# Kernel optimization log

Measured on AMD Instinct MI355X. Metric: run time of the kernel, lower is better.

The kernel has to match this reference:

```python
import jax, jax.numpy as jnp
import numpy as np
from jax import lax

NUM_CLASSES = 5
K_MAX = 5
PROTO_DIM = 32
MARGIN = 1.0
ANCHOR_STRENGTH = 1.0
LAMBDA_COMPACT = 0.1
MAX_ANCHORS = 2048
KMEANS_ITERS = 5
EPS = 1e-12


def _normalize(x, axis=-1):
    return x / jnp.sqrt(jnp.sum(x * x, axis=axis, keepdims=True) + EPS)


def _cdist(a, b):
    # Euclidean distance matrix (n, m) via the squared-norm expansion.
    d2 = (jnp.sum(a * a, 1)[:, None] + jnp.sum(b * b, 1)[None, :] - 2.0 * (a @ b.T))
    return jnp.sqrt(jnp.maximum(d2, 0.0))


def _class_centroids(feats, mask, key):
    # feats: (N, D) L2-normalized; mask: (N,) bool selecting this class's voxels.
    N, D = feats.shape
    w = mask.astype(feats.dtype)
    cnt = w.sum()
    mean = (feats * w[:, None]).sum(0) / jnp.maximum(cnt, 1.0)

    def kmeans(_):
        k_init, k_fb = jax.random.split(key)
        # random init: K distinct masked points (gumbel top-k == randperm sample)
        g0 = jax.random.gumbel(k_init, (N,))
        _, init_idx = lax.top_k(jnp.where(mask, g0, -jnp.inf), K_MAX)
        cent0 = feats[init_idx]
        # fallback random masked points for empty clusters, one set per iter
        g2 = jax.random.gumbel(k_fb, (KMEANS_ITERS, N))
        fb_idx = jax.vmap(lambda s: lax.top_k(jnp.where(mask, s, -jnp.inf), K_MAX)[1])(g2)

        def body(cent, fb):
            d = _cdist(feats, cent)                       # (N, K)
            assign = jnp.argmin(d, axis=1)
            onehot = ((assign[:, None] == jnp.arange(K_MAX)[None, :]) & mask[:, None]).astype(feats.dtype)
            counts = onehot.sum(0)                        # (K,)
            sums = onehot.T @ feats                       # (K, D)
            newc = sums / jnp.maximum(counts, 1.0)[:, None]
            newc = jnp.where(counts[:, None] > 0, newc, feats[fb])
            return newc, None

        cent, _ = lax.scan(body, cent0, fb_idx)
        return _normalize(cent)

    def mean_rep(_):
        return jnp.tile(mean[None, :], (K_MAX, 1))

    cent = lax.cond(cnt >= K_MAX, kmeans, mean_rep, None)
    return _normalize(cent), cnt


def _loss_triplet(feats, prototypes, pseudo_masks, gt_masks, labeled_batch):
    B, Df, Zf, Yf, Xf = feats.shape
    N = B * Zf * Yf * Xf
    feats_flat = _normalize(jnp.transpose(feats, (0, 2, 3, 4, 1)).reshape(N, Df))
    # masks are already at feature resolution -> nearest interp is identity
    gt_flat = gt_masks.reshape(-1)
    pseudo_flat = pseudo_masks.reshape(-1)
    protos = _normalize(prototypes)                       # (C, K, D)
    key = jax.random.key(42)

    # ---- anchor loss: match prototypes to per-class kmeans centroids ----
    anchor_loss = jnp.float32(0.0)
    anchor_cnt = jnp.float32(0.0)
    for i in range(int(labeled_batch.shape[0])):
        c = labeled_batch[i]
        c_safe = jnp.clip(c, 0, NUM_CLASSES - 1)
        cmask = gt_flat == c
        cent, cnt = _class_centroids(feats_flat, cmask, jax.random.fold_in(key, i))
        valid = ((c != 0) & (c < NUM_CLASSES) & (cnt > 0)).astype(jnp.float32)
        loss_c = jnp.mean((protos[c_safe] - cent) ** 2)
        anchor_loss = anchor_loss + valid * loss_c
        anchor_cnt = anchor_cnt + valid
    anchor_loss = anchor_loss / jnp.maximum(anchor_cnt, 1.0)

    # ---- compactness: unbiased variance across the K prototypes per class ----
    compact_loss = jnp.var(protos[1:], axis=1, ddof=1).mean(axis=1).sum()

    # ---- triplet loss over pseudo-labeled anchors ----
    amask = pseudo_flat > 0
    ga = jax.random.gumbel(jax.random.fold_in(key, 1000), (N,))
    top_s, aidx = lax.top_k(jnp.where(amask, ga, -jnp.inf), MAX_ANCHORS)
    sel_valid = jnp.isfinite(top_s)                        # padding if < MAX_ANCHORS anchors
    a_feats = feats_flat[aidx]                             # (A, D)
    a_labels = jnp.clip(pseudo_flat[aidx], 0, NUM_CLASSES - 1)

    CK = NUM_CLASSES * K_MAX
    protos_flat = protos.reshape(CK, Df)
    col_cls = jnp.arange(CK) // K_MAX
    own = col_cls[None, :] == a_labels[:, None]            # (A, CK)

    sim = a_feats @ protos_flat.T
    pos_idx = jnp.argmax(jnp.where(own, sim, -jnp.inf), axis=1)
    pos_vecs = protos_flat[pos_idx]

    d_all = _cdist(a_feats, protos_flat)                   # (A, CK)
    pos_d = jnp.min(jnp.where(own, d_all, jnp.inf), axis=1)
    neg = ~own
    semi = neg & (d_all > pos_d[:, None]) & (d_all < pos_d[:, None] + MARGIN)
    g1 = jax.random.gumbel(jax.random.fold_in(key, 2000), (MAX_ANCHORS, CK))
    g2 = jax.random.gumbel(jax.random.fold_in(key, 2001), (MAX_ANCHORS, CK))
    idx_semi = jnp.argmax(jnp.where(semi, g1, -jnp.inf), axis=1)
    idx_rand = jnp.argmax(jnp.where(neg, g2, -jnp.inf), axis=1)
    neg_idx = jnp.where(semi.any(axis=1), idx_semi, idx_rand)
    neg_vecs = protos_flat[neg_idx]

    aN, pN, nN = _normalize(a_feats), _normalize(pos_vecs), _normalize(neg_vecs)
    d_pos = jnp.sqrt(jnp.sum((aN - pN) ** 2, axis=1) + EPS)
    d_neg = jnp.sqrt(jnp.sum((aN - nN) ** 2, axis=1) + EPS)
    wA = (sel_valid & (a_labels != 0)).astype(jnp.float32)
    proto_loss = jnp.sum(jax.nn.softplus(d_pos - d_neg + MARGIN) * wA) / jnp.maximum(wA.sum(), 1.0)

    return proto_loss + ANCHOR_STRENGTH * anchor_loss + LAMBDA_COMPACT * compact_loss


def setup_inputs() -> dict:
    key = jax.random.key(0)
    k1, k2, k3, k4 = jax.random.split(key, 4)
    B, Z = 4, 64
    feats = jax.random.normal(k1, (B, PROTO_DIM, Z, Z, Z), dtype=jnp.float32)
    protos = jax.random.normal(k2, (NUM_CLASSES, K_MAX, PROTO_DIM), dtype=jnp.float32)
    protos = _normalize(protos)
    pseudo_masks = jax.random.randint(k3, (B, Z, Z, Z), 0, NUM_CLASSES, dtype=jnp.int32)
    gt_masks = jax.random.randint(k4, (B, Z, Z, Z), 0, NUM_CLASSES, dtype=jnp.int32)
    labeled_batch = jnp.array([1, 2, 3, 4], dtype=jnp.int32)
    return {"feats": feats, "prototypes": protos, "pseudo_masks": pseudo_masks,
            "gt_masks": gt_masks, "labeled_batch": labeled_batch}


def reference(feats, prototypes, pseudo_masks, gt_masks, labeled_batch):
    return _loss_triplet(feats, prototypes, pseudo_masks, gt_masks, labeled_batch)
```

## Files before the change

### kernel.cpp

```cpp
#include <hip/hip_runtime.h>
#include <stdint.h>

typedef unsigned int u32;
typedef unsigned long long u64;

#define NCLS 5
#define KMX 5
#define DD 32
#define LBN 4
#define KIT 5
#define MAXA 2048
#define CKK 25
#define NBLKA 256
#define SCPAD 36
#define PSTRIDE 680
#define ACAP 4096
#define UKTHR ((1u << 23) + 1u - (1u << 15))
#define FTINY 1.17549435e-38f

struct RKeys {
  u32 ki[LBN][2];
  u32 kf[LBN][2];
  u32 k1000[2];
  u32 k2000[2];
  u32 k2001[2];
};

struct SelState {
  u32 prefix1, rank1, prefix21, rank2, pivot_sv, target, M, ncand, ncand2;
};

__host__ __device__ inline void tf2x32(u32 k0, u32 k1, u32 x0, u32 x1, u32* o0, u32* o1) {
  u32 ks2 = k0 ^ k1 ^ 0x1BD11BDAu;
  u32 ks[3] = {k0, k1, ks2};
  x0 += k0; x1 += k1;
  const int rotA[4] = {13, 15, 26, 6};
  const int rotB[4] = {17, 29, 16, 24};
#pragma unroll
  for (int g = 0; g < 5; ++g) {
#pragma unroll
    for (int j = 0; j < 4; ++j) {
      int r = (g & 1) ? rotB[j] : rotA[j];
      x0 += x1;
      x1 = (x1 << r) | (x1 >> (32 - r));
      x1 ^= x0;
    }
    x0 += ks[(g + 1) % 3];
    x1 += ks[(g + 2) % 3] + (u32)(g + 1);
  }
  *o0 = x0; *o1 = x1;
}

__device__ inline u32 jax_ukey(u32 k0, u32 k1, u32 half, u32 idx) {
  bool hi = (idx >= half);
  u32 c0 = hi ? (idx - half) : idx;
  u32 c1 = hi ? idx : (idx + half);
  u32 o0, o1;
  tf2x32(k0, k1, c0, c1, &o0, &o1);
  u32 bits = hi ? o1 : o0;
  return (bits >> 9) + 1u;
}

#define INS5(kk, a0, a1, a2, a3, a4) do { u64 _k = (kk); \
  if (_k > a4) { a4 = _k; u64 _t; \
    if (a4 > a3) { _t = a3; a3 = a4; a4 = _t; } \
    if (a3 > a2) { _t = a2; a2 = a3; a3 = _t; } \
    if (a2 > a1) { _t = a1; a1 = a2; a2 = _t; } \
    if (a1 > a0) { _t = a0; a0 = a1; a1 = _t; } } } while (0)

#define WMERGE5(off, a0, a1, a2, a3, a4) do { \
  u64 r0 = __shfl_xor(a0, off, 64), r1 = __shfl_xor(a1, off, 64), \
      r2 = __shfl_xor(a2, off, 64), r3 = __shfl_xor(a3, off, 64), \
      r4 = __shfl_xor(a4, off, 64); \
  INS5(r0, a0, a1, a2, a3, a4); INS5(r1, a0, a1, a2, a3, a4); \
  INS5(r2, a0, a1, a2, a3, a4); INS5(r3, a0, a1, a2, a3, a4); \
  INS5(r4, a0, a1, a2, a3, a4); } while (0)

#define WMERGE_ALL(a0,a1,a2,a3,a4) do { \
  WMERGE5(32,a0,a1,a2,a3,a4); WMERGE5(16,a0,a1,a2,a3,a4); WMERGE5(8,a0,a1,a2,a3,a4); \
  WMERGE5(4,a0,a1,a2,a3,a4); WMERGE5(2,a0,a1,a2,a3,a4); WMERGE5(1,a0,a1,a2,a3,a4); } while (0)

__device__ inline float rsum32(float v) {
#pragma unroll
  for (int o = 16; o; o >>= 1) v += __shfl_xor(v, o, 32);
  return v;
}

__device__ inline float rsum64(float v) {
#pragma unroll
  for (int o = 32; o; o >>= 1) v += __shfl_xor(v, o, 64);
  return v;
}


__global__ void k_protos(const float* __restrict__ protos, float* __restrict__ protn, float* __restrict__ compact) {
  __shared__ float pl[CKK * DD];
  __shared__ float rn[CKK];
  __shared__ float red[4];
  int tid = threadIdx.x;
  for (int t = tid; t < CKK * DD; t += 256) pl[t] = protos[t];
  __syncthreads();
  if (tid < CKK) {
    float s = 0.f;
    for (int d = 0; d < DD; ++d) { float x = pl[tid * DD + d]; s += x * x; }
    rn[tid] = sqrtf(s + 1e-12f);
  }
  __syncthreads();
  for (int t = tid; t < CKK * DD; t += 256) {
    float v = pl[t] / rn[t / DD];
    pl[t] = v;
    protn[t] = v;
  }
  __syncthreads();
  float part = 0.f;
  if (tid < (NCLS - 1) * DD) {
    int c = 1 + tid / DD;
    int d = tid % DD;
    float m = 0.f;
#pragma unroll
    for (int k = 0; k < KMX; ++k) m += pl[(c * KMX + k) * DD + d];
    m *= (1.0f / KMX);
    float v = 0.f;
#pragma unroll
    for (int k = 0; k < KMX; ++k) { float df = pl[(c * KMX + k) * DD + d] - m; v += df * df; }
    part = v * (1.0f / (KMX - 1)) * (1.0f / DD);
  }
#pragma unroll
  for (int o = 32; o; o >>= 1) part += __shfl_xor(part, o, 64);
  int wid = tid >> 6;
  if ((tid & 63) == 0) red[wid] = part;
  __syncthreads();
  if (tid == 0) compact[0] = red[0] + red[1] + red[2] + red[3];
}


#define T5PROC_THR(gv_, nn_) do { \
  int ci = (gv_ == lb0) ? 0 : (gv_ == lb1) ? 1 : (gv_ == lb2) ? 2 : (gv_ == lb3) ? 3 : -1; \
  if (ci >= 0) { \
    u32 k0 = (ci & 2) ? ((ci & 1) ? ka3 : ka2) : ((ci & 1) ? ka1 : ka0); \
    u32 k1 = (ci & 2) ? ((ci & 1) ? kb3 : kb2) : ((ci & 1) ? kb1 : kb0); \
    u32 uk = jax_ukey(k0, k1, half, base + (u32)(nn_)); \
    if (uk >= UKTHR) { \
      u64 key = ((u64)uk << 32) | (u32)(~(u32)(nn_)); \
      if (ci == 0) { INS5(key, A0, A1, A2, A3, A4); } \
      else if (ci == 1) { INS5(key, B0, B1, B2, B3, B4); } \
      else if (ci == 2) { INS5(key, C0, C1, C2, C3, C4); } \
      else { INS5(key, D0, D1, D2, D3, D4); } \
    } \
  } } while (0)

#define T5PROC(gv_, nn_) do { \
  int ci = (gv_ == lb0) ? 0 : (gv_ == lb1) ? 1 : (gv_ == lb2) ? 2 : (gv_ == lb3) ? 3 : -1; \
  if (ci >= 0) { \
    u32 k0 = (ci & 2) ? ((ci & 1) ? ka3 : ka2) : ((ci & 1) ? ka1 : ka0); \
    u32 k1 = (ci & 2) ? ((ci & 1) ? kb3 : kb2) : ((ci & 1) ? kb1 : kb0); \
    u32 uk = jax_ukey(k0, k1, half, base + (u32)(nn_)); \
    u64 key = ((u64)uk << 32) | (u32)(~(u32)(nn_)); \
    if (ci == 0) { INS5(key, A0, A1, A2, A3, A4); } \
    else if (ci == 1) { INS5(key, B0, B1, B2, B3, B4); } \
    else if (ci == 2) { INS5(key, C0, C1, C2, C3, C4); } \
    else { INS5(key, D0, D1, D2, D3, D4); } \
  } } while (0)

#define T5_TAIL_STORE() \
  WMERGE_ALL(A0,A1,A2,A3,A4); \
  WMERGE_ALL(B0,B1,B2,B3,B4); \
  WMERGE_ALL(C0,C1,C2,C3,C4); \
  WMERGE_ALL(D0,D1,D2,D3,D4); \
  __shared__ u64 wbuf[4][20]; \
  int tid = threadIdx.x; \
  int wid = tid >> 6; \
  if ((tid & 63) == 0) { \
    u64* w = wbuf[wid]; \
    w[0]=A0; w[1]=A1; w[2]=A2; w[3]=A3; w[4]=A4; \
    w[5]=B0; w[6]=B1; w[7]=B2; w[8]=B3; w[9]=B4; \
    w[10]=C0; w[11]=C1; w[12]=C2; w[13]=C3; w[14]=C4; \
    w[15]=D0; w[16]=D1; w[17]=D2; w[18]=D3; w[19]=D4; \
  } \
  __syncthreads(); \
  if (tid == 0) { \
    _Pragma("unroll") \
    for (int w = 1; w < 4; ++w) { \
      _Pragma("unroll") \
      for (int j = 0; j < 5; ++j) { \
        u64 ka = wbuf[w][j];      INS5(ka, A0, A1, A2, A3, A4); \
        u64 kb = wbuf[w][5 + j];  INS5(kb, B0, B1, B2, B3, B4); \
        u64 kc = wbuf[w][10 + j]; INS5(kc, C0, C1, C2, C3, C4); \
        u64 kd = wbuf[w][15 + j]; INS5(kd, D0, D1, D2, D3, D4); \
      } \
    } \
    size_t nb = gridDim.x; \
    u64* o0 = outA + (((size_t)kind * LBN + 0) * nb + blockIdx.x) * 5; \
    o0[0]=A0; o0[1]=A1; o0[2]=A2; o0[3]=A3; o0[4]=A4; \
    u64* o1 = outA + (((size_t)kind * LBN + 1) * nb + blockIdx.x) * 5; \
    o1[0]=B0; o1[1]=B1; o1[2]=B2; o1[3]=B3; o1[4]=B4; \
    u64* o2 = outA + (((size_t)kind * LBN + 2) * nb + blockIdx.x) * 5; \
    o2[0]=C0; o2[1]=C1; o2[2]=C2; o2[3]=C3; o2[4]=C4; \
    u64* o3 = outA + (((size_t)kind * LBN + 3) * nb + blockIdx.x) * 5; \
    o3[0]=D0; o3[1]=D1; o3[2]=D2; o3[3]=D3; o3[4]=D4; \
  }

#define T5_HEAD() \
  int kind = blockIdx.y; \
  int lb0 = labeled[0], lb1 = labeled[1], lb2 = labeled[2], lb3 = labeled[3]; \
  u32 half = (kind == 0) ? (u32)(N / 2) : (u32)(((u64)5 * (u64)N) / 2); \
  u32 base = (kind == 0) ? 0u : (u32)((u64)(kind - 1) * (u64)N); \
  u32 ka0 = (kind == 0) ? RK.ki[0][0] : RK.kf[0][0], kb0 = (kind == 0) ? RK.ki[0][1] : RK.kf[0][1]; \
  u32 ka1 = (kind == 0) ? RK.ki[1][0] : RK.kf[1][0], kb1 = (kind == 0) ? RK.ki[1][1] : RK.kf[1][1]; \
  u32 ka2 = (kind == 0) ? RK.ki[2][0] : RK.kf[2][0], kb2 = (kind == 0) ? RK.ki[2][1] : RK.kf[2][1]; \
  u32 ka3 = (kind == 0) ? RK.ki[3][0] : RK.kf[3][0], kb3 = (kind == 0) ? RK.ki[3][1] : RK.kf[3][1]; \
  u64 A0=0,A1=0,A2=0,A3=0,A4=0; \
  u64 B0=0,B1=0,B2=0,B3=0,B4=0; \
  u64 C0=0,C1=0,C2=0,C3=0,C4=0; \
  u64 D0=0,D1=0,D2=0,D3=0,D4=0;

__global__ void k_top5A(const int* __restrict__ gt, const int* __restrict__ labeled,
                        RKeys RK, u64* __restrict__ outA, int N) {
  T5_HEAD()
  int Nq = N >> 2;
  int stride = gridDim.x * blockDim.x;
  for (int q = blockIdx.x * blockDim.x + threadIdx.x; q < Nq; q += stride) {
    int4 g4 = ((const int4*)gt)[q];
    int n = q << 2;
    T5PROC_THR(g4.x, n);
    T5PROC_THR(g4.y, n + 1);
    T5PROC_THR(g4.z, n + 2);
    T5PROC_THR(g4.w, n + 3);
  }
  T5_TAIL_STORE()
}

__global__ void k_top5B(const u64* __restrict__ outA, u32* __restrict__ rescue,
                        u64* __restrict__ top5F, int nblk) {
  int kind = blockIdx.x;
  int i = blockIdx.y;
  const u64* src = outA + ((size_t)kind * LBN + i) * nblk * 5;
  u64 t0 = 0, t1 = 0, t2 = 0, t3 = 0, t4 = 0;
  int tot = nblk * 5;
  for (int j = threadIdx.x; j < tot; j += blockDim.x) { u64 k = src[j]; INS5(k, t0, t1, t2, t3, t4); }
  WMERGE_ALL(t0, t1, t2, t3, t4);
  __shared__ u64 wbuf[4 * 5];
  int tid = threadIdx.x;
  int wid = tid >> 6;
  if ((tid & 63) == 0) {
    wbuf[wid * 5 + 0] = t0; wbuf[wid * 5 + 1] = t1; wbuf[wid * 5 + 2] = t2;
    wbuf[wid * 5 + 3] = t3; wbuf[wid * 5 + 4] = t4;
  }
  __syncthreads();
  if (tid == 0) {
#pragma unroll
    for (int w = 1; w < 4; ++w)
#pragma unroll
      for (int j = 0; j < 5; ++j) { u64 k = wbuf[w * 5 + j]; INS5(k, t0, t1, t2, t3, t4); }
    u64* o = top5F + ((size_t)kind * LBN + i) * 5;
    o[0] = t0; o[1] = t1; o[2] = t2; o[3] = t3; o[4] = t4;
    if (t4 == 0ULL) atomicOr(rescue, 1u << (kind * 4 + i));
  }
}

__global__ void k_top5A_resc(const int* __restrict__ gt, const int* __restrict__ labeled,
                             RKeys RK, const u32* __restrict__ rescue,
                             u64* __restrict__ outA, int N) {
  if (((rescue[0] >> (blockIdx.y * 4)) & 0xFu) == 0u) return;
  T5_HEAD()
  int Nq = N >> 2;
  int stride = gridDim.x * blockDim.x;
  for (int q = blockIdx.x * blockDim.x + threadIdx.x; q < Nq; q += stride) {
    int4 g4 = ((const int4*)gt)[q];
    int n = q << 2;
    T5PROC(g4.x, n);
    T5PROC(g4.y, n + 1);
    T5PROC(g4.z, n + 2);
    T5PROC(g4.w, n + 3);
  }
  T5_TAIL_STORE()
}

__global__ void k_top5B_resc(const u64* __restrict__ outA, const u32* __restrict__ rescue,
                             u64* __restrict__ top5F, int nblk) {
  int kind = blockIdx.x;
  int i = blockIdx.y;
  if (!((rescue[0] >> (kind * 4 + i)) & 1u)) return;
  const u64* src = outA + ((size_t)kind * LBN + i) * nblk * 5;
  u64 t0 = 0, t1 = 0, t2 = 0, t3 = 0, t4 = 0;
  int tot = nblk * 5;
  for (int j = threadIdx.x; j < tot; j += blockDim.x) { u64 k = src[j]; INS5(k, t0, t1, t2, t3, t4); }
  WMERGE_ALL(t0, t1, t2, t3, t4);
  __shared__ u64 wbuf[4 * 5];
  int tid = threadIdx.x;
  int wid = tid >> 6;
  if ((tid & 63) == 0) {
    wbuf[wid * 5 + 0] = t0; wbuf[wid * 5 + 1] = t1; wbuf[wid * 5 + 2] = t2;
    wbuf[wid * 5 + 3] = t3; wbuf[wid * 5 + 4] = t4;
  }
  __syncthreads();
  if (tid == 0) {
#pragma unroll
    for (int w = 1; w < 4; ++w)
#pragma unroll
      for (int j = 0; j < 5; ++j) { u64 k = wbuf[w * 5 + j]; INS5(k, t0, t1, t2, t3, t4); }
    u64* o = top5F + ((size_t)kind * LBN + i) * 5;
    o[0] = t0; o[1] = t1; o[2] = t2; o[3] = t3; o[4] = t4;
  }
}


__global__ void __launch_bounds__(256)
k_normT(const float* __restrict__ feats, float4* __restrict__ featsN4, int N, int Z3) {
  __shared__ float xl[256 * 33];
  __shared__ float sinv[256];
  int tid = threadIdx.x;
  int nchunk = N >> 8;
  for (int chunk = blockIdx.x; chunk < nchunk; chunk += gridDim.x) {
    int n0 = chunk << 8;
    int b = n0 / Z3, v0 = n0 - b * Z3;
    const float* fp = feats + (size_t)b * DD * Z3 + v0 + tid;
#pragma unroll
    for (int d = 0; d < DD; ++d) xl[tid * 33 + d] = fp[(size_t)d * Z3];
    float s = 0.f;
#pragma unroll
    for (int d = 0; d < DD; ++d) { float x = xl[tid * 33 + d]; s += x * x; }
    sinv[tid] = 1.0f / sqrtf(s + 1e-12f);
    __syncthreads();
#pragma unroll
    for (int i = 0; i < 8; ++i) {
      int fi = i * 256 + tid;
      int vox = fi >> 3, q = fi & 7;
      float iv = sinv[vox];
      float4 o;
      o.x = xl[vox * 33 + q * 4 + 0] * iv;
      o.y = xl[vox * 33 + q * 4 + 1] * iv;
      o.z = xl[vox * 33 + q * 4 + 2] * iv;
      o.w = xl[vox * 33 + q * 4 + 3] * iv;
      featsN4[(size_t)n0 * 8 + fi] = o;
    }
    __syncthreads();
  }
}

__global__ void k_initcentT(const float* __restrict__ featsN,
                            const u64* __restrict__ top5F, float* __restrict__ cent, int N) {
  int t = threadIdx.x;
  if (t >= LBN * KMX * DD) return;
  int d = t & 31;
  int k = (t >> 5) % KMX;
  int i = t / (KMX * DD);
  u32 n = ~(u32)(top5F[((size_t)0 * LBN + i) * 5 + k]);
  if (n >= (u32)N) n = 0;
  cent[(i * KMX + k) * DD + d] = featsN[(size_t)n * DD + d];
}

__global__ void __launch_bounds__(256)
k_assignW2(const float4* __restrict__ featsN4, const int* __restrict__ gt,
           const int* __restrict__ labeled, const float* __restrict__ cent,
           float* __restrict__ part, int N) {
  __shared__ float sc[LBN * KMX * SCPAD];
  __shared__ float ssw[8][LBN * KMX * SCPAD];
  __shared__ float scn[LBN * KMX];
  __shared__ float scw[8][LBN * KMX];
  int tid = threadIdx.x;
  for (int t = tid; t < LBN * KMX * DD; t += 256) {
    int cl2 = t >> 5, d = t & 31;
    sc[cl2 * SCPAD + d] = cent[t];
  }
  for (int t = tid; t < 8 * LBN * KMX * SCPAD; t += 256) (&ssw[0][0])[t] = 0.f;
  for (int t = tid; t < 8 * LBN * KMX; t += 256) (&scw[0][0])[t] = 0.f;
  __syncthreads();
  if (tid < LBN * KMX) {
    float s = 0.f;
#pragma unroll
    for (int d = 0; d < DD; ++d) { float c = sc[tid * SCPAD + d]; s += c * c; }
    scn[tid] = s;
  }
  __syncthreads();
  int lb0 = labeled[0], lb1 = labeled[1], lb2 = labeled[2], lb3 = labeled[3];
  int q = tid & 7;
  int grp = (tid >> 3) & 7;
  int wv = tid >> 6;
  int cpi = 2 * wv + (grp >> 2);
  float* myss = &ssw[cpi][0];
  float* mysc = &scw[cpi][0];
  int sstep = grp & 3;
  const float* scq = sc + q * 4;
  int nchunk = N >> 5;
  int chunk = blockIdx.x;
  if (chunk < nchunk) {
    float4 f4 = featsN4[(size_t)chunk * 256 + tid];
    int g = gt[(chunk << 5) + (tid >> 3)];
    while (true) {
      int nxt = chunk + gridDim.x;
      bool has = nxt < nchunk;
      float4 nf4; int ng = 0;
      if (has) {
        nf4 = featsN4[(size_t)nxt * 256 + tid];
        ng = gt[(nxt << 5) + (tid >> 3)];
      }
      int ci = (g == lb0) ? 0 : (g == lb1) ? 1 : (g == lb2) ? 2 : (g == lb3) ? 3 : -1;
      int basec = (ci < 0 ? 0 : ci) * KMX;
      float4 c0 = *(const float4*)(scq + (basec + 0) * SCPAD);
      float4 c1 = *(const float4*)(scq + (basec + 1) * SCPAD);
      float4 c2 = *(const float4*)(scq + (basec + 2) * SCPAD);
      float4 c3 = *(const float4*)(scq + (basec + 3) * SCPAD);
      float4 c4 = *(const float4*)(scq + (basec + 4) * SCPAD);
      float p0 = f4.x * c0.x + f4.y * c0.y + f4.z * c0.z + f4.w * c0.w;
      float p1 = f4.x * c1.x + f4.y * c1.y + f4.z * c1.z + f4.w * c1.w;
      float p2 = f4.x * c2.x + f4.y * c2.y + f4.z * c2.z + f4.w * c2.w;
      float p3 = f4.x * c3.x + f4.y * c3.y + f4.z * c3.z + f4.w * c3.w;
      float p4 = f4.x * c4.x + f4.y * c4.y + f4.z * c4.z + f4.w * c4.w;
#pragma unroll
      for (int o = 1; o < 8; o <<= 1) {
        p0 += __shfl_xor(p0, o, 64);
        p1 += __shfl_xor(p1, o, 64);
        p2 += __shfl_xor(p2, o, 64);
        p3 += __shfl_xor(p3, o, 64);
        p4 += __shfl_xor(p4, o, 64);
      }
      float bd = scn[basec + 0] - 2.0f * p0; int bk = 0;
      float d2;
      d2 = scn[basec + 1] - 2.0f * p1; if (d2 < bd) { bd = d2; bk = 1; }
      d2 = scn[basec + 2] - 2.0f * p2; if (d2 < bd) { bd = d2; bk = 2; }
      d2 = scn[basec + 3] - 2.0f * p3; if (d2 < bd) { bd = d2; bk = 3; }
      d2 = scn[basec + 4] - 2.0f * p4; if (d2 < bd) { bd = d2; bk = 4; }
      int cl = basec + bk;
#pragma unroll
      for (int s = 0; s < 4; ++s) {
        if (sstep == s && ci >= 0) {
          float* dst = myss + cl * SCPAD + q * 4;
          float4 cur = *(float4*)dst;
          cur.x += f4.x; cur.y += f4.y; cur.z += f4.z; cur.w += f4.w;
          *(float4*)dst = cur;
          if (q == 0) mysc[cl] += 1.0f;
        }
      }
      if (!has) break;
      chunk = nxt; f4 = nf4; g = ng;
    }
  }
  __syncthreads();
  float* po = part + (size_t)blockIdx.x * PSTRIDE;
  for (int p = tid; p < 660; p += 256) {
    float v;
    if (p < 640) {
      int idx = (p >> 5) * SCPAD + (p & 31);
      v = ssw[0][idx] + ssw[1][idx] + ssw[2][idx] + ssw[3][idx]
        + ssw[4][idx] + ssw[5][idx] + ssw[6][idx] + ssw[7][idx];
    } else {
      int ik = p - 640;
      v = scw[0][ik] + scw[1][ik] + scw[2][ik] + scw[3][ik]
        + scw[4][ik] + scw[5][ik] + scw[6][ik] + scw[7][ik];
    }
    po[p] = v;
  }
}

__global__ void k_redupdT(const float* __restrict__ part, const float* __restrict__ featsN,
                          const u64* __restrict__ top5F, float* __restrict__ cent,
                          float* __restrict__ sums, float* __restrict__ kcnt,
                          int iter, int N, int NB) {
  __shared__ float w4[8];
  int p = blockIdx.x;
  int tid = threadIdx.x;
  if (p < 640) {
    int ik = p >> 5, d = p & 31;
    float s = 0.f, c = 0.f;
    for (int b2 = tid; b2 < NB; b2 += 256) {
      s += part[(size_t)b2 * PSTRIDE + p];
      c += part[(size_t)b2 * PSTRIDE + 640 + ik];
    }
    s = rsum64(s); c = rsum64(c);
    int wid = tid >> 6;
    if ((tid & 63) == 0) { w4[wid] = s; w4[4 + wid] = c; }
    __syncthreads();
    if (tid == 0) {
      float S = w4[0] + w4[1] + w4[2] + w4[3];
      float C = w4[4] + w4[5] + w4[6] + w4[7];
      sums[p] = S;
      if (C > 0.f) {
        cent[p] = S / fmaxf(C, 1.0f);
      } else {
        int i = ik / KMX, k = ik % KMX;
        u32 n = ~(u32)(top5F[((size_t)(1 + iter) * LBN + i) * 5 + k]);
        if (n >= (u32)N) n = 0;
        cent[p] = featsN[(size_t)n * DD + d];
      }
    }
  } else if (p < 660) {
    int ik = p - 640;
    float c = 0.f;
    for (int b2 = tid; b2 < NB; b2 += 256) c += part[(size_t)b2 * PSTRIDE + 640 + ik];
    c = rsum64(c);
    int wid = tid >> 6;
    if ((tid & 63) == 0) w4[wid] = c;
    __syncthreads();
    if (tid == 0) kcnt[ik] = w4[0] + w4[1] + w4[2] + w4[3];
  }
}

__global__ void k_prepT(const float4* __restrict__ featsN4,
                        const int* __restrict__ pseudo, const SelState* __restrict__ st,
                        const int* __restrict__ aidx, float4* __restrict__ afe4,
                        int* __restrict__ alab, int N) {
  int tid = threadIdx.x;
  int r = blockIdx.x * 32 + (tid >> 3);
  int q = tid & 7;
  if (r >= (int)st->target) return;
  int n = aidx[r];
  if ((u32)n >= (u32)N) n = 0;
  if (q == 0) {
    int lb = pseudo[n];
    alab[r] = lb < 0 ? 0 : (lb > NCLS - 1 ? NCLS - 1 : lb);
  }
  afe4[(size_t)r * 8 + q] = featsN4[(size_t)n * 8 + q];
}


__global__ void __launch_bounds__(256)
k_anchsel(const int* __restrict__ pseudo, RKeys RK, u64* __restrict__ cand4k,
          SelState* st, int N) {
  __shared__ u32 mcnt[4];
  u32 K0 = RK.k1000[0], K1 = RK.k1000[1];
  u32 half = (u32)(N / 2);
  int tid = threadIdx.x;
  int lcnt = 0;
  int stride = gridDim.x * blockDim.x;
  for (int n = blockIdx.x * blockDim.x + tid; n < N; n += stride) {
    bool valid = pseudo[n] > 0;
    lcnt += valid ? 1 : 0;
    u32 uk = jax_ukey(K0, K1, half, (u32)n);
    bool c = valid && (uk >= UKTHR);
    if (__ballot(c)) {
      if (c) {
        u32 p = atomicAdd(&st->ncand, 1u);
        if (p < (u32)ACAP) cand4k[p] = ((u64)uk << 32) | (u32)(~(u32)n);
      }
    }
  }
#pragma unroll
  for (int o = 32; o; o >>= 1) lcnt += __shfl_xor(lcnt, o, 64);
  if ((tid & 63) == 0) mcnt[tid >> 6] = (u32)lcnt;
  __syncthreads();
  if (tid == 0) atomicAdd(&st->M, mcnt[0] + mcnt[1] + mcnt[2] + mcnt[3]);
}

__global__ void k_selmode(SelState* st, u32* rescue) {
  if (threadIdx.x != 0 || blockIdx.x != 0) return;
  u32 M = st->M;
  u32 tgt = M < (u32)MAXA ? M : (u32)MAXA;
  st->target = tgt;
  if (!(st->ncand >= tgt && st->ncand <= (u32)ACAP)) rescue[1] = 1u;
}

__global__ void __launch_bounds__(256)
k_rank(const u64* __restrict__ cand4k, const SelState* __restrict__ st,
       const u32* __restrict__ rescue, int* __restrict__ aidx) {
  if (rescue[1]) return;
  __shared__ u64 keys[ACAP];
  u32 nc = st->ncand; if (nc > (u32)ACAP) nc = (u32)ACAP;
  u32 target = st->target;
  int tid = threadIdx.x;
  for (int t = tid; t < ACAP; t += 256) keys[t] = (t < (int)nc) ? cand4k[t] : 0ULL;
  __syncthreads();
  int i = blockIdx.x * 256 + tid;
  if (i >= (int)nc) return;
  u64 my = keys[i];
  u32 rank = 0;
  for (u32 j = 0; j < nc; ++j) rank += (keys[j] > my) ? 1u : 0u;
  if (rank < target) aidx[rank] = (int)(~(u32)my);
}


__global__ void k_svinit(const int* __restrict__ pseudo, RKeys RK, const u32* __restrict__ rescue,
                         u32* __restrict__ sv, u32* __restrict__ hist, int N) {
  if (!rescue[1]) return;
  __shared__ u32 h[2048];
  for (int t = threadIdx.x; t < 2048; t += blockDim.x) h[t] = 0;
  __syncthreads();
  u32 half = (u32)(N / 2);
  u32 K0 = RK.k1000[0], K1 = RK.k1000[1];
  int Nq = N >> 2;
  int stride = gridDim.x * blockDim.x;
  for (int q = blockIdx.x * blockDim.x + threadIdx.x; q < Nq; q += stride) {
    int4 p4 = ((const int4*)pseudo)[q];
    int n = q << 2;
    u32 s0 = 0, s1 = 0, s2 = 0, s3 = 0;
    if (p4.x > 0) { s0 = jax_ukey(K0, K1, half, (u32)n);     atomicAdd(&h[s0 >> 21], 1u); }
    if (p4.y > 0) { s1 = jax_ukey(K0, K1, half, (u32)n + 1); atomicAdd(&h[s1 >> 21], 1u); }
    if (p4.z > 0) { s2 = jax_ukey(K0, K1, half, (u32)n + 2); atomicAdd(&h[s2 >> 21], 1u); }
    if (p4.w > 0) { s3 = jax_ukey(K0, K1, half, (u32)n + 3); atomicAdd(&h[s3 >> 21], 1u); }
    ((uint4*)sv)[q] = make_uint4(s0, s1, s2, s3);
  }
  __syncthreads();
  for (int t = threadIdx.x; t < 2048; t += blockDim.x) if (h[t]) atomicAdd(&hist[t], h[t]);
}

__global__ void k_hist12(const u32* __restrict__ sv, u32* __restrict__ hist,
                         const SelState* __restrict__ st, const u32* __restrict__ rescue,
                         int pass, int N) {
  if (!rescue[1]) return;
  __shared__ u32 h[2048];
  for (int t = threadIdx.x; t < 2048; t += blockDim.x) h[t] = 0;
  __syncthreads();
  u32 pre = (pass == 1) ? st->prefix1 : st->prefix21;
  int Nq = N >> 2;
  int stride = gridDim.x * blockDim.x;
  for (int q = blockIdx.x * blockDim.x + threadIdx.x; q < Nq; q += stride) {
    uint4 s4 = ((const uint4*)sv)[q];
#define H12(s_) do { u32 s = (s_); if (s) { \
      if (pass == 1) { if ((s >> 21) == pre) atomicAdd(&h[(s >> 10) & 0x7FFu], 1u); } \
      else           { if ((s >> 10) == pre) atomicAdd(&h[s & 0x3FFu], 1u); } } } while (0)
    H12(s4.x); H12(s4.y); H12(s4.z); H12(s4.w);
#undef H12
  }
  __syncthreads();
  for (int t = threadIdx.x; t < 2048; t += blockDim.x) if (h[t]) atomicAdd(&hist[t], h[t]);
}

__global__ void k_scan(const u32* __restrict__ hist, SelState* st,
                       const u32* __restrict__ rescue, int pass) {
  if (!rescue[1]) return;
  __shared__ u32 h[2048];
  __shared__ u32 csum[256];
  __shared__ u32 sh_rank;
  __shared__ int sh_found;
  __shared__ u32 sh_rem;
  int tid = threadIdx.x;
  int nb = (pass == 2) ? 1024 : 2048;
  for (int t = tid; t < 2048; t += 256) h[t] = (t < nb) ? hist[t] : 0u;
  __syncthreads();
  u32 cs = 0;
#pragma unroll
  for (int j = 0; j < 8; ++j) cs += h[tid * 8 + j];
  csum[tid] = cs;
  __syncthreads();
  if (tid == 0) {
    sh_rank = (pass == 0) ? st->target : (pass == 1 ? st->rank1 : st->rank2);
    sh_found = -1;
    sh_rem = 0;
  }
  __syncthreads();
  u32 rank = sh_rank;
  if (rank > 0) {
    u32 above = 0;
    for (int j = tid + 1; j < 256; ++j) above += csum[j];
    u32 run = above;
    for (int b = tid * 8 + 7; b >= tid * 8; --b) {
      u32 c = h[b];
      if (run < rank && rank <= run + c) { sh_found = b; sh_rem = rank - run; }
      run += c;
    }
  }
  __syncthreads();
  if (tid == 0) {
    int found = sh_found;
    u32 rem = sh_rem;
    if (pass == 0) {
      if (found < 0) { st->prefix1 = 0xFFFFFFFFu; st->rank1 = 0; }
      else { st->prefix1 = (u32)found; st->rank1 = rem; }
    } else if (pass == 1) {
      if (found < 0) { st->prefix21 = 0xFFFFFFFFu; st->rank2 = 0; }
      else { st->prefix21 = (st->prefix1 << 11) | (u32)found; st->rank2 = rem; }
    } else {
      if (found < 0) st->pivot_sv = 0xFFFFFFFFu;
      else st->pivot_sv = (st->prefix21 << 10) | (u32)found;
    }
  }
}

__global__ void k_gather(const u32* __restrict__ sv, SelState* st,
                         const u32* __restrict__ rescue, u64* __restrict__ cand, int N) {
  if (!rescue[1]) return;
  if (st->target == 0) return;
  u32 piv = st->pivot_sv;
  int Nq = N >> 2;
  int stride = gridDim.x * blockDim.x;
  for (int q = blockIdx.x * blockDim.x + threadIdx.x; q < Nq; q += stride) {
    uint4 s4 = ((const uint4*)sv)[q];
    int n = q << 2;
#define GPUSH(s_, nn_) do { u32 s = (s_); \
    if (s && s >= piv) { u32 p = atomicAdd(&st->ncand2, 1u); \
      if (p < 4096u) cand[p] = ((u64)s << 32) | (u32)(~(u32)(nn_)); } } while (0)
    GPUSH(s4.x, n); GPUSH(s4.y, n + 1); GPUSH(s4.z, n + 2); GPUSH(s4.w, n + 3);
#undef GPUSH
  }
}

__global__ void __launch_bounds__(1024) k_sortsel(const u64* __restrict__ cand,
                                                  const SelState* __restrict__ st,
                                                  const u32* __restrict__ rescue,
                                                  int* __restrict__ aidx) {
  if (!rescue[1]) return;
  __shared__ u64 s[4096];
  u32 nc = st->ncand2; if (nc > 4096u) nc = 4096u;
  u32 target = st->target;
  for (int t = threadIdx.x; t < 4096; t += blockDim.x) s[t] = (t < (int)nc) ? cand[t] : 0ULL;
  __syncthreads();
  for (u32 ksz = 2; ksz <= 4096; ksz <<= 1) {
    for (u32 j = ksz >> 1; j > 0; j >>= 1) {
      for (u32 idx = threadIdx.x; idx < 4096; idx += blockDim.x) {
        u32 ixj = idx ^ j;
        if (ixj > idx) {
          bool up = (idx & ksz) == 0;
          u64 A = s[idx], B = s[ixj];
          bool sw = up ? (A < B) : (A > B);
          if (sw) { s[idx] = B; s[ixj] = A; }
        }
      }
      __syncthreads();
    }
  }
  for (int t = threadIdx.x; t < MAXA; t += blockDim.x)
    if (t < (int)target) aidx[t] = (int)(~(u32)s[t]);
}


__global__ void k_anchor_final(const float* __restrict__ cent, const float* __restrict__ sums,
                               const float* __restrict__ kcnt, const float* __restrict__ protn,
                               const int* __restrict__ labeled, float* __restrict__ accum) {
  int i = blockIdx.x;
  int d = threadIdx.x;
  if (d >= DD) return;
  int c = labeled[i];
  float cnt = 0.f;
#pragma unroll
  for (int k = 0; k < KMX; ++k) cnt += kcnt[i * KMX + k];
  int cs = c < 0 ? 0 : (c > NCLS - 1 ? NCLS - 1 : c);
  float part = 0.f;
  if (cnt >= (float)KMX) {
#pragma unroll
    for (int k = 0; k < KMX; ++k) {
      float v = cent[(i * KMX + k) * DD + d];
      float s = rsum32(v * v);
      float dn1 = sqrtf(s + 1e-12f);
      float v1 = v / dn1;
      float s2 = rsum32(v1 * v1);
      float dn2 = sqrtf(s2 + 1e-12f);
      float vv = v1 / dn2;
      float df = protn[(cs * KMX + k) * DD + d] - vv;
      part += df * df;
    }
  } else {
    float mv = 0.f;
#pragma unroll
    for (int k = 0; k < KMX; ++k) mv += sums[(i * KMX + k) * DD + d];
    mv /= fmaxf(cnt, 1.0f);
    float s = rsum32(mv * mv);
    float dn = sqrtf(s + 1e-12f);
    float vv = mv / dn;
#pragma unroll
    for (int k = 0; k < KMX; ++k) {
      float df = protn[(cs * KMX + k) * DD + d] - vv;
      part += df * df;
    }
  }
  float ls = rsum32(part) * (1.0f / (KMX * DD));
  bool valid = (c != 0) && (c < NCLS) && (cnt > 0.f);
  if (d == 0 && valid) { atomicAdd(&accum[0], ls); atomicAdd(&accum[1], 1.0f); }
}

__global__ void k_triplet(const float* __restrict__ protn, const float* __restrict__ afe,
                          const int* __restrict__ alab, const SelState* __restrict__ st,
                          RKeys RK, float* __restrict__ acc) {
  __shared__ float pn[CKK * DD];
  __shared__ float spn[CKK];
  int tid = threadIdx.x;
  for (int t = tid; t < CKK * DD; t += blockDim.x) pn[t] = protn[t];
  __syncthreads();
  if (tid < CKK) {
    float s = 0.f;
    for (int d = 0; d < DD; ++d) s += pn[tid * DD + d] * pn[tid * DD + d];
    spn[tid] = s;
  }
  __syncthreads();
  int r = blockIdx.x * blockDim.x + tid;
  if (r >= (int)st->target) return;
  float a[DD]; float sa = 0.f;
#pragma unroll
  for (int d = 0; d < DD; ++d) { a[d] = afe[(size_t)r * DD + d]; sa += a[d] * a[d]; }
  int lab = alab[r];
  int ob = lab * KMX;
  float bs = -3.4e38f; int pidx = ob;
  float pos_d = 3.4e38f;
  for (int k = ob; k < ob + KMX; ++k) {
    float dot = 0.f;
#pragma unroll
    for (int d = 0; d < DD; ++d) dot += a[d] * pn[k * DD + d];
    if (dot > bs) { bs = dot; pidx = k; }
    float d2 = (sa + spn[k]) - 2.0f * dot;
    float dd = sqrtf(fmaxf(d2, 0.f));
    pos_d = fminf(pos_d, dd);
  }
  u32 halfT = (u32)(MAXA * CKK / 2);
  bool any_semi = false;
  u32 bu1 = 0; int k1i = 0;
  u32 bu2 = 0; int k2i = 0;
  for (int k = 0; k < CKK; ++k) {
    if (k / KMX == lab) continue;
    float dot = 0.f;
#pragma unroll
    for (int d = 0; d < DD; ++d) dot += a[d] * pn[k * DD + d];
    float d2 = (sa + spn[k]) - 2.0f * dot;
    float dd = sqrtf(fmaxf(d2, 0.f));
    u32 j = (u32)(r * CKK + k);
    bool semi = (dd > pos_d) && (dd < pos_d + 1.0f);
    if (semi) {
      u32 u1 = jax_ukey(RK.k2000[0], RK.k2000[1], halfT, j);
      any_semi = true;
      if (u1 > bu1) { bu1 = u1; k1i = k; }
    }
    u32 u2 = jax_ukey(RK.k2001[0], RK.k2001[1], halfT, j);
    if (u2 > bu2) { bu2 = u2; k2i = k; }
  }
  int nidx = any_semi ? k1i : k2i;
  float aden = sqrtf(sa + 1e-12f);
  float pden = sqrtf(spn[pidx] + 1e-12f);
  float nden = sqrtf(spn[nidx] + 1e-12f);
  float s1 = 0.f, s2 = 0.f;
#pragma unroll
  for (int d = 0; d < DD; ++d) {
    float an = a[d] / aden;
    float pv = pn[pidx * DD + d] / pden;
    float nv = pn[nidx * DD + d] / nden;
    float t1 = an - pv; s1 += t1 * t1;
    float t2 = an - nv; s2 += t2 * t2;
  }
  float d_pos = sqrtf(s1 + 1e-12f);
  float d_neg = sqrtf(s2 + 1e-12f);
  float xx = (d_pos - d_neg) + 1.0f;
  float l = fmaxf(xx, 0.f) + log1pf(expf(-fabsf(xx)));
  atomicAdd(&acc[0], l);
  atomicAdd(&acc[1], 1.0f);
}

__global__ void k_final(const float* __restrict__ anchor_acc, const float* __restrict__ proto_acc,
                        const float* __restrict__ compact, float* __restrict__ out) {
  if (threadIdx.x != 0 || blockIdx.x != 0) return;
  float al = anchor_acc[0] / fmaxf(anchor_acc[1], 1.0f);
  float pl = proto_acc[0] / fmaxf(proto_acc[1], 1.0f);
  out[0] = pl + 1.0f * al + 0.1f * compact[0];
}


static void host_keys(RKeys* K) {
  const u32 b0 = 0u, b1 = 42u;
  u32 o0, o1;
  for (int i = 0; i < LBN; ++i) {
    u32 f0, f1;
    tf2x32(b0, b1, 0u, (u32)i, &f0, &f1);
    u32 p0, q0, p1, q1;
    tf2x32(f0, f1, 0u, 2u, &p0, &q0);
    tf2x32(f0, f1, 1u, 3u, &p1, &q1);
    K->ki[i][0] = p0; K->ki[i][1] = p1;
    K->kf[i][0] = q0; K->kf[i][1] = q1;
  }
  tf2x32(b0, b1, 0u, 1000u, &o0, &o1); K->k1000[0] = o0; K->k1000[1] = o1;
  tf2x32(b0, b1, 0u, 2000u, &o0, &o1); K->k2000[0] = o0; K->k2000[1] = o1;
  tf2x32(b0, b1, 0u, 2001u, &o0, &o1); K->k2001[0] = o0; K->k2001[1] = o1;
}

extern "C" void kernel_launch(void* const* d_in, const int* in_sizes, int n_in,
                              void* d_out, int out_size, void* d_ws, size_t ws_size,
                              hipStream_t stream) {
  const float* feats = (const float*)d_in[0];
  const float* protos = (const float*)d_in[1];
  const int* pseudo = (const int*)d_in[2];
  const int* gt = (const int*)d_in[3];
  const int* labeled = (const int*)d_in[4];
  float* out = (float*)d_out;

  int N = in_sizes[2];
  int Z3 = N / 4;

  RKeys RK;
  host_keys(&RK);

  const int nbas[3] = {1280, 640, 320};
  for (int attempt = 0; attempt < 3; ++attempt) {
    int NBAS = nbas[attempt];
    char* W = (char*)d_ws;
    size_t off = 0;
    auto alloc = [&](size_t bytes) -> char* {
      char* p = W + off;
      off += (bytes + 255) & ~(size_t)255;
      return p;
    };
    char* zeroBase = W + off;
    u32* hist3 = (u32*)alloc(3 * 2048 * 4);
    SelState* st = (SelState*)alloc(256);
    float* anchor_acc = (float*)alloc(256);
    float* proto_acc = (float*)alloc(256);
    u32* rescue = (u32*)alloc(256);
    size_t zeroBytes = (size_t)((W + off) - zeroBase);
    u64* cand4k = (u64*)alloc((size_t)ACAP * 8);
    u64* outA = (u64*)alloc((size_t)6 * LBN * NBLKA * 5 * 8);
    u64* top5F = (u64*)alloc((size_t)6 * LBN * 5 * 8);
    float* cent = (float*)alloc((size_t)LBN * KMX * DD * 4);
    float* sums = (float*)alloc((size_t)LBN * KMX * DD * 4);
    float* kcnt = (float*)alloc((size_t)LBN * KMX * 4);
    float* protn = (float*)alloc((size_t)CKK * DD * 4);
    float* compact = (float*)alloc(256);
    u32* sv = (u32*)alloc((size_t)N * 4);
    float* part = (float*)alloc((size_t)NBAS * PSTRIDE * 4);
    u64* cand = (u64*)alloc(4096 * 8);
    int* aidx = (int*)alloc((size_t)MAXA * 4);
    int* alab = (int*)alloc((size_t)MAXA * 4);
    float* afe = (float*)alloc((size_t)MAXA * DD * 4);
    float* featsN = (float*)alloc((size_t)N * DD * 4);
    if (ws_size < off) continue;

    hipMemsetAsync(zeroBase, 0, zeroBytes, stream);

    k_protos<<<dim3(1), dim3(256), 0, stream>>>(protos, protn, compact);

    k_top5A<<<dim3(NBLKA, 6), dim3(256), 0, stream>>>(gt, labeled, RK, outA, N);
    k_top5B<<<dim3(6, LBN), dim3(256), 0, stream>>>(outA, rescue, top5F, NBLKA);
    k_top5A_resc<<<dim3(NBLKA, 6), dim3(256), 0, stream>>>(gt, labeled, RK, rescue, outA, N);
    k_top5B_resc<<<dim3(6, LBN), dim3(256), 0, stream>>>(outA, rescue, top5F, NBLKA);

    float4* featsN4 = (float4*)featsN;
    k_normT<<<dim3(2048), dim3(256), 0, stream>>>(feats, featsN4, N, Z3);
    k_initcentT<<<dim3(1), dim3(LBN * KMX * DD), 0, stream>>>(featsN, top5F, cent, N);
    for (int it = 0; it < KIT; ++it) {
      k_assignW2<<<dim3(NBAS), dim3(256), 0, stream>>>(featsN4, gt, labeled, cent, part, N);
      k_redupdT<<<dim3(660), dim3(256), 0, stream>>>(part, featsN, top5F, cent, sums, kcnt, it, N, NBAS);
    }
    k_anchor_final<<<dim3(LBN), dim3(64), 0, stream>>>(cent, sums, kcnt, protn, labeled, anchor_acc);

    k_anchsel<<<dim3(2048), dim3(256), 0, stream>>>(pseudo, RK, cand4k, st, N);
    k_selmode<<<dim3(1), dim3(64), 0, stream>>>(st, rescue);
    k_svinit<<<dim3(1024), dim3(256), 0, stream>>>(pseudo, RK, rescue, sv, hist3, N);
    k_scan<<<dim3(1), dim3(256), 0, stream>>>(hist3, st, rescue, 0);
    k_hist12<<<dim3(1024), dim3(256), 0, stream>>>(sv, hist3 + 2048, st, rescue, 1, N);
    k_scan<<<dim3(1), dim3(256), 0, stream>>>(hist3 + 2048, st, rescue, 1);
    k_hist12<<<dim3(1024), dim3(256), 0, stream>>>(sv, hist3 + 4096, st, rescue, 2, N);
    k_scan<<<dim3(1), dim3(256), 0, stream>>>(hist3 + 4096, st, rescue, 2);
    k_gather<<<dim3(1024), dim3(256), 0, stream>>>(sv, st, rescue, cand, N);
    k_sortsel<<<dim3(1), dim3(1024), 0, stream>>>(cand, st, rescue, aidx);
    k_rank<<<dim3(ACAP / 256), dim3(256), 0, stream>>>(cand4k, st, rescue, aidx);

    k_prepT<<<dim3(MAXA / 32), dim3(256), 0, stream>>>(featsN4, pseudo, st, aidx,
                                                        (float4*)afe, alab, N);
    k_triplet<<<dim3(MAXA / 256), dim3(256), 0, stream>>>(protn, afe, alab, st, RK, proto_acc);

    k_final<<<dim3(1), dim3(64), 0, stream>>>(anchor_acc, proto_acc, compact, out);
    return;
  }
}
```

Baseline: 614.3 us.

## Compute k-means fallback top-5 lazily only when a cluster goes empty

Drops the eager computation of fallback random top-5 indices for all five k-means iterations, which had five extra grid rows scanning the full label volume. Empty clusters are now flagged via an atomic mask, and a single-block k_fixempty kernel computes the fallback indices for the affected classes only when needed. The normalization transpose kernel is retiled to 128-voxel chunks with coalesced loads, and the assign partial-block counts are raised. The lazy path adds one small kernel launch per iteration and would be slow if empty clusters actually occur, since one block then scans all N voxels.

Result: faster. 600.3 us (-2.3%).

```diff
diff --git a/kernel.cpp b/kernel.cpp
--- a/kernel.cpp
+++ b/kernel.cpp
@@ -139,7 +139,7 @@
   if (ci >= 0) { \
     u32 k0 = (ci & 2) ? ((ci & 1) ? ka3 : ka2) : ((ci & 1) ? ka1 : ka0); \
     u32 k1 = (ci & 2) ? ((ci & 1) ? kb3 : kb2) : ((ci & 1) ? kb1 : kb0); \
-    u32 uk = jax_ukey(k0, k1, half, base + (u32)(nn_)); \
+    u32 uk = jax_ukey(k0, k1, half, (u32)(nn_)); \
     if (uk >= UKTHR) { \
       u64 key = ((u64)uk << 32) | (u32)(~(u32)(nn_)); \
       if (ci == 0) { INS5(key, A0, A1, A2, A3, A4); } \
@@ -154,7 +154,7 @@
   if (ci >= 0) { \
     u32 k0 = (ci & 2) ? ((ci & 1) ? ka3 : ka2) : ((ci & 1) ? ka1 : ka0); \
     u32 k1 = (ci & 2) ? ((ci & 1) ? kb3 : kb2) : ((ci & 1) ? kb1 : kb0); \
-    u32 uk = jax_ukey(k0, k1, half, base + (u32)(nn_)); \
+    u32 uk = jax_ukey(k0, k1, half, (u32)(nn_)); \
     u64 key = ((u64)uk << 32) | (u32)(~(u32)(nn_)); \
     if (ci == 0) { INS5(key, A0, A1, A2, A3, A4); } \
     else if (ci == 1) { INS5(key, B0, B1, B2, B3, B4); } \
@@ -190,25 +190,23 @@
       } \
     } \
     size_t nb = gridDim.x; \
-    u64* o0 = outA + (((size_t)kind * LBN + 0) * nb + blockIdx.x) * 5; \
+    u64* o0 = outA + ((size_t)0 * nb + blockIdx.x) * 5; \
     o0[0]=A0; o0[1]=A1; o0[2]=A2; o0[3]=A3; o0[4]=A4; \
-    u64* o1 = outA + (((size_t)kind * LBN + 1) * nb + blockIdx.x) * 5; \
+    u64* o1 = outA + ((size_t)1 * nb + blockIdx.x) * 5; \
     o1[0]=B0; o1[1]=B1; o1[2]=B2; o1[3]=B3; o1[4]=B4; \
-    u64* o2 = outA + (((size_t)kind * LBN + 2) * nb + blockIdx.x) * 5; \
+    u64* o2 = outA + ((size_t)2 * nb + blockIdx.x) * 5; \
     o2[0]=C0; o2[1]=C1; o2[2]=C2; o2[3]=C3; o2[4]=C4; \
-    u64* o3 = outA + (((size_t)kind * LBN + 3) * nb + blockIdx.x) * 5; \
+    u64* o3 = outA + ((size_t)3 * nb + blockIdx.x) * 5; \
     o3[0]=D0; o3[1]=D1; o3[2]=D2; o3[3]=D3; o3[4]=D4; \
   }
 
 #define T5_HEAD() \
-  int kind = blockIdx.y; \
   int lb0 = labeled[0], lb1 = labeled[1], lb2 = labeled[2], lb3 = labeled[3]; \
-  u32 half = (kind == 0) ? (u32)(N / 2) : (u32)(((u64)5 * (u64)N) / 2); \
-  u32 base = (kind == 0) ? 0u : (u32)((u64)(kind - 1) * (u64)N); \
-  u32 ka0 = (kind == 0) ? RK.ki[0][0] : RK.kf[0][0], kb0 = (kind == 0) ? RK.ki[0][1] : RK.kf[0][1]; \
-  u32 ka1 = (kind == 0) ? RK.ki[1][0] : RK.kf[1][0], kb1 = (kind == 0) ? RK.ki[1][1] : RK.kf[1][1]; \
-  u32 ka2 = (kind == 0) ? RK.ki[2][0] : RK.kf[2][0], kb2 = (kind == 0) ? RK.ki[2][1] : RK.kf[2][1]; \
-  u32 ka3 = (kind == 0) ? RK.ki[3][0] : RK.kf[3][0], kb3 = (kind == 0) ? RK.ki[3][1] : RK.kf[3][1]; \
+  u32 half = (u32)(N / 2); \
+  u32 ka0 = RK.ki[0][0], kb0 = RK.ki[0][1]; \
+  u32 ka1 = RK.ki[1][0], kb1 = RK.ki[1][1]; \
+  u32 ka2 = RK.ki[2][0], kb2 = RK.ki[2][1]; \
+  u32 ka3 = RK.ki[3][0], kb3 = RK.ki[3][1]; \
   u64 A0=0,A1=0,A2=0,A3=0,A4=0; \
   u64 B0=0,B1=0,B2=0,B3=0,B4=0; \
   u64 C0=0,C1=0,C2=0,C3=0,C4=0; \
@@ -232,9 +230,8 @@
 
 __global__ void k_top5B(const u64* __restrict__ outA, u32* __restrict__ rescue,
                         u64* __restrict__ top5F, int nblk) {
-  int kind = blockIdx.x;
-  int i = blockIdx.y;
-  const u64* src = outA + ((size_t)kind * LBN + i) * nblk * 5;
+  int i = blockIdx.x;
+  const u64* src = outA + (size_t)i * nblk * 5;
   u64 t0 = 0, t1 = 0, t2 = 0, t3 = 0, t4 = 0;
   int tot = nblk * 5;
   for (int j = threadIdx.x; j < tot; j += blockDim.x) { u64 k = src[j]; INS5(k, t0, t1, t2, t3, t4); }
@@ -252,16 +249,16 @@
     for (int w = 1; w < 4; ++w)
 #pragma unroll
       for (int j = 0; j < 5; ++j) { u64 k = wbuf[w * 5 + j]; INS5(k, t0, t1, t2, t3, t4); }
-    u64* o = top5F + ((size_t)kind * LBN + i) * 5;
+    u64* o = top5F + (size_t)i * 5;
     o[0] = t0; o[1] = t1; o[2] = t2; o[3] = t3; o[4] = t4;
-    if (t4 == 0ULL) atomicOr(rescue, 1u << (kind * 4 + i));
+    if (t4 == 0ULL) atomicOr(rescue, 1u << i);
   }
 }
 
 __global__ void k_top5A_resc(const int* __restrict__ gt, const int* __restrict__ labeled,
                              RKeys RK, const u32* __restrict__ rescue,
                              u64* __restrict__ outA, int N) {
-  if (((rescue[0] >> (blockIdx.y * 4)) & 0xFu) == 0u) return;
+  if ((rescue[0] & 0xFu) == 0u) return;
   T5_HEAD()
   int Nq = N >> 2;
   int stride = gridDim.x * blockDim.x;
@@ -278,10 +275,9 @@
 
 __global__ void k_top5B_resc(const u64* __restrict__ outA, const u32* __restrict__ rescue,
                              u64* __restrict__ top5F, int nblk) {
-  int kind = blockIdx.x;
-  int i = blockIdx.y;
-  if (!((rescue[0] >> (kind * 4 + i)) & 1u)) return;
-  const u64* src = outA + ((size_t)kind * LBN + i) * nblk * 5;
+  int i = blockIdx.x;
+  if (!((rescue[0] >> i) & 1u)) return;
+  const u64* src = outA + (size_t)i * nblk * 5;
   u64 t0 = 0, t1 = 0, t2 = 0, t3 = 0, t4 = 0;
   int tot = nblk * 5;
   for (int j = threadIdx.x; j < tot; j += blockDim.x) { u64 k = src[j]; INS5(k, t0, t1, t2, t3, t4); }
@@ -299,7 +295,7 @@
     for (int w = 1; w < 4; ++w)
 #pragma unroll
       for (int j = 0; j < 5; ++j) { u64 k = wbuf[w * 5 + j]; INS5(k, t0, t1, t2, t3, t4); }
-    u64* o = top5F + ((size_t)kind * LBN + i) * 5;
+    u64* o = top5F + (size_t)i * 5;
     o[0] = t0; o[1] = t1; o[2] = t2; o[3] = t3; o[4] = t4;
   }
 }
@@ -307,32 +303,39 @@
 
 __global__ void __launch_bounds__(256)
 k_normT(const float* __restrict__ feats, float4* __restrict__ featsN4, int N, int Z3) {
-  __shared__ float xl[256 * 33];
-  __shared__ float sinv[256];
-  int tid = threadIdx.x;
-  int nchunk = N >> 8;
+  __shared__ float xl[128 * 33];
+  __shared__ float sinv[128];
+  int tid = threadIdx.x;
+  int nchunk = N >> 7;
   for (int chunk = blockIdx.x; chunk < nchunk; chunk += gridDim.x) {
-    int n0 = chunk << 8;
+    int n0 = chunk << 7;
     int b = n0 / Z3, v0 = n0 - b * Z3;
-    const float* fp = feats + (size_t)b * DD * Z3 + v0 + tid;
-#pragma unroll
-    for (int d = 0; d < DD; ++d) xl[tid * 33 + d] = fp[(size_t)d * Z3];
-    float s = 0.f;
-#pragma unroll
-    for (int d = 0; d < DD; ++d) { float x = xl[tid * 33 + d]; s += x * x; }
-    sinv[tid] = 1.0f / sqrtf(s + 1e-12f);
+    const float* fb = feats + (size_t)b * DD * Z3 + v0;
+#pragma unroll
+    for (int j = 0; j < 16; ++j) {
+      int idx = j * 256 + tid;
+      int d = idx >> 7, v = idx & 127;
+      xl[v * 33 + d] = fb[(size_t)d * Z3 + v];
+    }
     __syncthreads();
-#pragma unroll
-    for (int i = 0; i < 8; ++i) {
-      int fi = i * 256 + tid;
-      int vox = fi >> 3, q = fi & 7;
+    if (tid < 128) {
+      float s = 0.f;
+#pragma unroll
+      for (int d = 0; d < DD; ++d) { float x = xl[tid * 33 + d]; s += x * x; }
+      sinv[tid] = 1.0f / sqrtf(s + 1e-12f);
+    }
+    __syncthreads();
+#pragma unroll
+    for (int j = 0; j < 4; ++j) {
+      int idx = j * 256 + tid;
+      int vox = idx >> 3, q = idx & 7;
       float iv = sinv[vox];
       float4 o;
       o.x = xl[vox * 33 + q * 4 + 0] * iv;
       o.y = xl[vox * 33 + q * 4 + 1] * iv;
       o.z = xl[vox * 33 + q * 4 + 2] * iv;
       o.w = xl[vox * 33 + q * 4 + 3] * iv;
-      featsN4[(size_t)n0 * 8 + fi] = o;
+      featsN4[(size_t)n0 * 8 + idx] = o;
     }
     __syncthreads();
   }
@@ -345,7 +348,7 @@
   int d = t & 31;
   int k = (t >> 5) % KMX;
   int i = t / (KMX * DD);
-  u32 n = ~(u32)(top5F[((size_t)0 * LBN + i) * 5 + k]);
+  u32 n = ~(u32)(top5F[(size_t)i * 5 + k]);
   if (n >= (u32)N) n = 0;
   cent[(i * KMX + k) * DD + d] = featsN[(size_t)n * DD + d];
 }
@@ -453,15 +456,14 @@
   }
 }
 
-__global__ void k_redupdT(const float* __restrict__ part, const float* __restrict__ featsN,
-                          const u64* __restrict__ top5F, float* __restrict__ cent,
+__global__ void k_redupdT(const float* __restrict__ part, float* __restrict__ cent,
                           float* __restrict__ sums, float* __restrict__ kcnt,
-                          int iter, int N, int NB) {
+                          u32* __restrict__ emptyMask, int NB) {
   __shared__ float w4[8];
   int p = blockIdx.x;
   int tid = threadIdx.x;
   if (p < 640) {
-    int ik = p >> 5, d = p & 31;
+    int ik = p >> 5;
     float s = 0.f, c = 0.f;
     for (int b2 = tid; b2 < NB; b2 += 256) {
       s += part[(size_t)b2 * PSTRIDE + p];
@@ -475,14 +477,8 @@
       float S = w4[0] + w4[1] + w4[2] + w4[3];
       float C = w4[4] + w4[5] + w4[6] + w4[7];
       sums[p] = S;
-      if (C > 0.f) {
-        cent[p] = S / fmaxf(C, 1.0f);
-      } else {
-        int i = ik / KMX, k = ik % KMX;
-        u32 n = ~(u32)(top5F[((size_t)(1 + iter) * LBN + i) * 5 + k]);
-        if (n >= (u32)N) n = 0;
-        cent[p] = featsN[(size_t)n * DD + d];
-      }
+      if (C > 0.f) cent[p] = S / fmaxf(C, 1.0f);
+      else atomicOr(emptyMask, 1u << ik);
     }
   } else if (p < 660) {
     int ik = p - 640;
@@ -494,6 +490,55 @@
     __syncthreads();
     if (tid == 0) kcnt[ik] = w4[0] + w4[1] + w4[2] + w4[3];
   }
+}
+
+__global__ void __launch_bounds__(1024)
+k_fixempty(const float* __restrict__ featsN, const int* __restrict__ gt,
+           const int* __restrict__ labeled, RKeys RK, u32* __restrict__ emptyMask,
+           float* __restrict__ cent, int iter, int N) {
+  u32 mask = emptyMask[0];
+  if (mask == 0u) return;
+  __shared__ u64 wbuf[16 * 5];
+  __shared__ u32 idxs[KMX];
+  int tid = threadIdx.x;
+  u32 halfF = (u32)(((u64)5 * (u64)N) / 2);
+  for (int ci = 0; ci < LBN; ++ci) {
+    if (((mask >> (ci * KMX)) & 0x1Fu) == 0u) continue;
+    int c = labeled[ci];
+    u32 fa = RK.kf[ci][0], fb = RK.kf[ci][1];
+    u32 base = (u32)iter * (u32)N;
+    u64 t0 = 0, t1 = 0, t2 = 0, t3 = 0, t4 = 0;
+    for (int n = tid; n < N; n += 1024) {
+      if (gt[n] != c) continue;
+      u32 uk = jax_ukey(fa, fb, halfF, base + (u32)n);
+      u64 key = ((u64)uk << 32) | (u32)(~(u32)n);
+      INS5(key, t0, t1, t2, t3, t4);
+    }
+    WMERGE_ALL(t0, t1, t2, t3, t4);
+    int wid = tid >> 6;
+    if ((tid & 63) == 0) {
+      wbuf[wid * 5 + 0] = t0; wbuf[wid * 5 + 1] = t1; wbuf[wid * 5 + 2] = t2;
+      wbuf[wid * 5 + 3] = t3; wbuf[wid * 5 + 4] = t4;
+    }
+    __syncthreads();
+    if (tid == 0) {
+      for (int w = 1; w < 16; ++w)
+        for (int j = 0; j < 5; ++j) { u64 k = wbuf[w * 5 + j]; INS5(k, t0, t1, t2, t3, t4); }
+      idxs[0] = ~(u32)t0; idxs[1] = ~(u32)t1; idxs[2] = ~(u32)t2;
+      idxs[3] = ~(u32)t3; idxs[4] = ~(u32)t4;
+    }
+    __syncthreads();
+    if (tid < KMX * DD) {
+      int k = tid >> 5, d = tid & 31;
+      if ((mask >> (ci * KMX + k)) & 1u) {
+        u32 n = idxs[k];
+        if (n >= (u32)N) n = 0;
+        cent[(ci * KMX + k) * DD + d] = featsN[(size_t)n * DD + d];
+      }
+    }
+    __syncthreads();
+  }
+  if (tid == 0) emptyMask[0] = 0u;
 }
 
 __global__ void k_prepT(const float4* __restrict__ featsN4,
@@ -873,7 +918,7 @@
   RKeys RK;
   host_keys(&RK);
 
-  const int nbas[3] = {1280, 640, 320};
+  const int nbas[3] = {1536, 768, 384};
   for (int attempt = 0; attempt < 3; ++attempt) {
     int NBAS = nbas[attempt];
     char* W = (char*)d_ws;
@@ -891,8 +936,8 @@
     u32* rescue = (u32*)alloc(256);
     size_t zeroBytes = (size_t)((W + off) - zeroBase);
     u64* cand4k = (u64*)alloc((size_t)ACAP * 8);
-    u64* outA = (u64*)alloc((size_t)6 * LBN * NBLKA * 5 * 8);
-    u64* top5F = (u64*)alloc((size_t)6 * LBN * 5 * 8);
+    u64* outA = (u64*)alloc((size_t)LBN * NBLKA * 5 * 8);
+    u64* top5F = (u64*)alloc((size_t)LBN * 5 * 8);
     float* cent = (float*)alloc((size_t)LBN * KMX * DD * 4);
     float* sums = (float*)alloc((size_t)LBN * KMX * DD * 4);
     float* kcnt = (float*)alloc((size_t)LBN * KMX * 4);
@@ -911,17 +956,18 @@
 
     k_protos<<<dim3(1), dim3(256), 0, stream>>>(protos, protn, compact);
 
-    k_top5A<<<dim3(NBLKA, 6), dim3(256), 0, stream>>>(gt, labeled, RK, outA, N);
-    k_top5B<<<dim3(6, LBN), dim3(256), 0, stream>>>(outA, rescue, top5F, NBLKA);
-    k_top5A_resc<<<dim3(NBLKA, 6), dim3(256), 0, stream>>>(gt, labeled, RK, rescue, outA, N);
-    k_top5B_resc<<<dim3(6, LBN), dim3(256), 0, stream>>>(outA, rescue, top5F, NBLKA);
+    k_top5A<<<dim3(NBLKA), dim3(256), 0, stream>>>(gt, labeled, RK, outA, N);
+    k_top5B<<<dim3(LBN), dim3(256), 0, stream>>>(outA, rescue, top5F, NBLKA);
+    k_top5A_resc<<<dim3(NBLKA), dim3(256), 0, stream>>>(gt, labeled, RK, rescue, outA, N);
+    k_top5B_resc<<<dim3(LBN), dim3(256), 0, stream>>>(outA, rescue, top5F, NBLKA);
 
     float4* featsN4 = (float4*)featsN;
-    k_normT<<<dim3(2048), dim3(256), 0, stream>>>(feats, featsN4, N, Z3);
+    k_normT<<<dim3(4096), dim3(256), 0, stream>>>(feats, featsN4, N, Z3);
     k_initcentT<<<dim3(1), dim3(LBN * KMX * DD), 0, stream>>>(featsN, top5F, cent, N);
     for (int it = 0; it < KIT; ++it) {
       k_assignW2<<<dim3(NBAS), dim3(256), 0, stream>>>(featsN4, gt, labeled, cent, part, N);
-      k_redupdT<<<dim3(660), dim3(256), 0, stream>>>(part, featsN, top5F, cent, sums, kcnt, it, N, NBAS);
+      k_redupdT<<<dim3(660), dim3(256), 0, stream>>>(part, cent, sums, kcnt, rescue + 2, NBAS);
+      k_fixempty<<<dim3(1), dim3(1024), 0, stream>>>(featsN, gt, labeled, RK, rescue + 2, cent, it, N);
     }
     k_anchor_final<<<dim3(LBN), dim3(64), 0, stream>>>(cent, sums, kcnt, protn, labeled, anchor_acc);
 
```
